# Kernel optimization log

Measured on AMD Instinct MI355X. Metric: run time of the kernel, lower is better.

The kernel has to match this reference:

```python
import jax, jax.numpy as jnp
import numpy as np

B, L = 1024, 50
H = 512
N_ITEM, N_ENTITY, N_WORD = 50000, 100000, 30000


def setup_inputs() -> dict:
    key = jax.random.key(0)
    ks = jax.random.split(key, 16)
    inp = {
        "item_ids": jax.random.randint(ks[0], (B, L), 0, N_ITEM),
        "item_len": jax.random.randint(ks[1], (B,), 0, 51),
        "entity_ids": jax.random.randint(ks[2], (B, L), 0, N_ENTITY),
        "entity_len": jax.random.randint(ks[3], (B,), 0, 51),
        "word_ids": jax.random.randint(ks[4], (B, L), 0, N_WORD),
        "word_len": jax.random.randint(ks[5], (B,), 0, 51),
        "labels": jax.random.randint(ks[6], (B,), 0, N_ITEM),
        # learned parameters (torch default-ish init scales)
        "item_emb": jax.random.normal(ks[7], (N_ITEM, H), jnp.float32),
        "entity_emb": jax.random.normal(ks[8], (N_ENTITY, H), jnp.float32),
        "word_emb": jax.random.normal(ks[9], (N_WORD, H), jnp.float32),
        "W1": jax.random.normal(ks[10], (H, 4 * H), jnp.float32) / np.sqrt(H),
        "b1": jnp.zeros((4 * H,), jnp.float32),
        "W2": jax.random.normal(ks[11], (4 * H, N_ITEM), jnp.float32) / np.sqrt(4 * H),
        "b2": jnp.zeros((N_ITEM,), jnp.float32),
    }
    return inp


def _masked_mean(table, ids, lens):
    # segment-mean over ragged lists encoded as padded ids + lengths.
    # empty list -> zeros (matches the torch zero-fallback branch).
    mask = (jnp.arange(L)[None, :] < lens[:, None]).astype(table.dtype)  # [B,L]
    emb = table[ids]                                                     # [B,L,H]
    s = jnp.einsum("blh,bl->bh", emb, mask)
    denom = jnp.maximum(lens, 1).astype(table.dtype)[:, None]
    return s / denom


def reference(item_emb, entity_emb, word_emb, W1, b1, W2, b2,
              item_ids, item_len, entity_ids, entity_len,
              word_ids, word_len, labels):
    u = (_masked_mean(item_emb, item_ids, item_len)
         + _masked_mean(entity_emb, entity_ids, entity_len)
         + _masked_mean(word_emb, word_ids, word_len)) / 3.0   # [B,H]
    h = jax.nn.relu(u @ W1 + b1)                                # [B,4H]
    probs = jax.nn.softmax(h @ W2 + b2, axis=-1)                # [B,n_item]
    # faithful to source: CrossEntropyLoss applied on top of softmax outputs
    logp = jax.nn.log_softmax(probs, axis=-1)
    loss = -jnp.mean(jnp.take_along_axis(logp, labels[:, None], axis=-1))
    return probs, labels, loss
```

## Files before the change

### kernel.cpp

```cpp
#include <hip/hip_runtime.h>
#include <cstdint>
#include <cstddef>

typedef __attribute__((ext_vector_type(8))) short bf16x8;
typedef __attribute__((ext_vector_type(4))) float f32x4;

#define B_DIM 1024
#define L_SEQ 50
#define H_DIM 512
#define NITEM 50000
#define PSTRIDE 400

__device__ __forceinline__ unsigned short f2bf(float x) {
  unsigned u = __float_as_uint(x);
  return (unsigned short)((u + 0x7fffu + ((u >> 16) & 1u)) >> 16);
}
__device__ __forceinline__ unsigned pack2(float lo, float hi) {
  return (unsigned)f2bf(lo) | ((unsigned)f2bf(hi) << 16);
}
__device__ __forceinline__ void gld16(const unsigned short* g, unsigned short* l) {
  __builtin_amdgcn_global_load_lds((const __attribute__((address_space(1))) void*)g,
                                   (__attribute__((address_space(3))) void*)l, 16, 0, 0);
}
#define BAR() asm volatile("s_barrier" ::: "memory")

__device__ __forceinline__ void mean_body(int b2, const int* __restrict__ item_ids,
                                          const int* __restrict__ item_len,
                                          const int* __restrict__ ent_ids,
                                          const int* __restrict__ ent_len,
                                          const int* __restrict__ word_ids,
                                          const int* __restrict__ word_len,
                                          const float* __restrict__ item_emb,
                                          const float* __restrict__ ent_emb,
                                          const float* __restrict__ word_emb,
                                          unsigned short* __restrict__ u_bf) {
  const int b = b2 >> 1;
  const int col = ((b2 & 1) << 8) + threadIdx.x;
  float out = 0.f;
  {
    const int len = item_len[b]; float a = 0.f;
#pragma unroll 4
    for (int l = 0; l < len; ++l) a += item_emb[(size_t)item_ids[b * L_SEQ + l] * H_DIM + col];
    out += a / (float)(len > 0 ? len : 1);
  }
  {
    const int len = ent_len[b]; float a = 0.f;
#pragma unroll 4
    for (int l = 0; l < len; ++l) a += ent_emb[(size_t)ent_ids[b * L_SEQ + l] * H_DIM + col];
    out += a / (float)(len > 0 ? len : 1);
  }
  {
    const int len = word_len[b]; float a = 0.f;
#pragma unroll 4
    for (int l = 0; l < len; ++l) a += word_emb[(size_t)word_ids[b * L_SEQ + l] * H_DIM + col];
    out += a / (float)(len > 0 ? len : 1);
  }
  u_bf[b * H_DIM + col] = f2bf(out / 3.f);
}

__global__ void mean_kernel(const int* __restrict__ item_ids, const int* __restrict__ item_len,
                            const int* __restrict__ ent_ids, const int* __restrict__ ent_len,
                            const int* __restrict__ word_ids, const int* __restrict__ word_len,
                            const float* __restrict__ item_emb, const float* __restrict__ ent_emb,
                            const float* __restrict__ word_emb, unsigned short* __restrict__ u_bf) {
  mean_body(blockIdx.x, item_ids, item_len, ent_ids, ent_len, word_ids, word_len, item_emb,
            ent_emb, word_emb, u_bf);
}

__device__ __forceinline__ void transpose_body(const float* __restrict__ W,
                                               unsigned short* __restrict__ Wt, int K, int N,
                                               int k0, int n0, float (*tile)[65]) {
  const int tn = threadIdx.x & 63, tk = threadIdx.x >> 6;
  const int nv = (n0 + tn < N) ? n0 + tn : N - 1;
#pragma unroll
  for (int i = 0; i < 16; ++i)
    tile[tk + 4 * i][tn] = W[(size_t)(k0 + tk + 4 * i) * N + nv];
  __syncthreads();
  const int rn = threadIdx.x >> 2, ck = (threadIdx.x & 3) * 16;
  if (n0 + rn < N) {
    uint4 o[2];
    unsigned* po = (unsigned*)&o[0];
#pragma unroll
    for (int c = 0; c < 8; ++c)
      po[c] = pack2(tile[ck + 2 * c][rn], tile[ck + 2 * c + 1][rn]);
    *(uint4*)&Wt[(size_t)(n0 + rn) * K + k0 + ck] = o[0];
    *(uint4*)&Wt[(size_t)(n0 + rn) * K + k0 + ck + 8] = o[1];
  }
}

__global__ void prep_kernel(const int* __restrict__ item_ids, const int* __restrict__ item_len,
                            const int* __restrict__ ent_ids, const int* __restrict__ ent_len,
                            const int* __restrict__ word_ids, const int* __restrict__ word_len,
                            const float* __restrict__ item_emb, const float* __restrict__ ent_emb,
                            const float* __restrict__ word_emb, unsigned short* __restrict__ u_bf,
                            const float* __restrict__ W1, unsigned short* __restrict__ W1t,
                            const float* __restrict__ W2, unsigned short* __restrict__ W2t) {
  __shared__ float tile[64][65];
  const int b = blockIdx.x;
  if (b < 2048) {
    mean_body(b, item_ids, item_len, ent_ids, ent_len, word_ids, word_len, item_emb, ent_emb,
              word_emb, u_bf);
  } else if (b < 2048 + 25024) {
    const int t = b - 2048;
    transpose_body(W2, W2t, 2048, NITEM, (t & 31) * 64, (t >> 5) * 64, tile);
  } else {
    const int t = b - (2048 + 25024);
    transpose_body(W1, W1t, 512, 2048, (t & 7) * 64, (t >> 3) * 64, tile);
  }
}

template <int K, int N>
__global__ void transpose_bf16(const float* __restrict__ W, unsigned short* __restrict__ Wt) {
  __shared__ float tile[64][65];
  transpose_body(W, Wt, K, N, blockIdx.x * 64, blockIdx.y * 64, tile);
}

template <int K, int N, int EPI>
__global__ __launch_bounds__(512, 1) void gemm128x256(const unsigned short* __restrict__ Ag,
                                                      const unsigned short* __restrict__ Btg,
                                                      const float* __restrict__ bias,
                                                      unsigned short* __restrict__ Cbf,
                                                      float* __restrict__ Cf,
                                                      float* __restrict__ pmax,
                                                      float* __restrict__ psum) {
  __shared__ unsigned short lds[4 * 4096 + 4 * 8192];
  unsigned short* Aring = lds;
  unsigned short* Bring = lds + 4 * 4096;

  const int tid = threadIdx.x;
  const int lane = tid & 63;
  const int wid = tid >> 6;

  const int nwg = gridDim.x;
  const int wgid = (blockIdx.x & 7) * (nwg >> 3) + (blockIdx.x >> 3);
  const int m0 = (wgid & 7) * 128;
  const int panel = wgid >> 3;
  const int n0 = panel * 256;

  const int cg = (lane & 3) ^ ((lane >> 3) & 3);
  const int arow = wid * 16 + (lane >> 2);
  const unsigned short* pa = Ag + (size_t)(m0 + arow) * K + cg * 8;
  const int br0 = wid * 32 + (lane >> 2), br1 = br0 + 16;
  int rg0 = n0 + br0; rg0 = rg0 < N ? rg0 : N - 1;
  int rg1 = n0 + br1; rg1 = rg1 < N ? rg1 : N - 1;
  const unsigned short* pb0 = Btg + (size_t)rg0 * K + cg * 8;
  const unsigned short* pb1 = Btg + (size_t)rg1 * K + cg * 8;
  const int li0 = wid * 2, li1 = wid * 2 + 1;

  const int wr = wid >> 2, wc = wid & 3;
  const int l15 = lane & 15, kb = lane >> 4;
  f32x4 acc[4][4] = {};

  const int HS = K / 32;
#pragma unroll
  for (int hh = 0; hh < 3; ++hh) {
    const int ko = hh * 32;
    gld16(pa + ko, &Aring[hh * 4096 + wid * 512]);
    gld16(pb0 + ko, &Bring[hh * 8192 + li0 * 512]);
    gld16(pb1 + ko, &Bring[hh * 8192 + li1 * 512]);
  }
  asm volatile("s_waitcnt vmcnt(6)" ::: "memory");
  BAR();

#pragma unroll 1
  for (int h = 0; h < HS; ++h) {
    const int slot = h & 3;
    const int nslot = (h + 3) & 3;
    const int kst = (h + 3) * 32;
    const unsigned short* As_ = &Aring[slot * 4096];
    const unsigned short* Bs_ = &Bring[slot * 8192];

    if (h + 3 < HS) {
      gld16(pa + kst, &Aring[nslot * 4096 + wid * 512]);
      gld16(pb0 + kst, &Bring[nslot * 8192 + li0 * 512]);
      gld16(pb1 + kst, &Bring[nslot * 8192 + li1 * 512]);
    }

    bf16x8 af[4], bf[4];
#pragma unroll
    for (int i = 0; i < 4; ++i) {
      const int row = wr * 64 + i * 16 + l15;
      af[i] = *(const bf16x8*)&As_[row * 32 + (kb ^ ((row >> 1) & 3)) * 8];
    }
#pragma unroll
    for (int j = 0; j < 4; ++j) {
      const int col = wc * 64 + j * 16 + l15;
      bf[j] = *(const bf16x8*)&Bs_[col * 32 + (kb ^ ((col >> 1) & 3)) * 8];
    }
    __builtin_amdgcn_s_setprio(1);
#pragma unroll
    for (int i = 0; i < 4; ++i)
#pragma unroll
      for (int j = 0; j < 4; ++j)
        acc[i][j] = __builtin_amdgcn_mfma_f32_16x16x32_bf16(af[i], bf[j], acc[i][j], 0, 0, 0);
    __builtin_amdgcn_s_setprio(0);

    if (h + 1 < HS) {
      if (h + 4 <= HS)
        asm volatile("s_waitcnt vmcnt(6)" ::: "memory");
      else if (h + 3 == HS)
        asm volatile("s_waitcnt vmcnt(3)" ::: "memory");
      else
        asm volatile("s_waitcnt vmcnt(0)" ::: "memory");
      BAR();
    }
  }

  float bv[4];
  bool val[4];
#pragma unroll
  for (int j = 0; j < 4; ++j) {
    const int cgl = n0 + wc * 64 + 16 * j + l15;
    val[j] = (cgl < N);
    bv[j] = bias[val[j] ? cgl : 0];
  }
#pragma unroll
  for (int i = 0; i < 4; ++i) {
    const int rbase = m0 + wr * 64 + 16 * i + 4 * kb;
#pragma unroll
    for (int j = 0; j < 4; ++j) {
      if (val[j]) {
        const int cgl = n0 + wc * 64 + 16 * j + l15;
#pragma unroll
        for (int rr = 0; rr < 4; ++rr) {
          const float v = acc[i][j][rr] + bv[j];
          if (EPI == 0)
            Cbf[(size_t)(rbase + rr) * N + cgl] = f2bf(v > 0.f ? v : 0.f);
          else
            Cf[(size_t)(rbase + rr) * N + cgl] = v;
        }
      }
    }
  }

  if constexpr (EPI == 1) {
    __syncthreads();
    float* redm = (float*)&lds[0];
    float* reds = redm + 512;
#pragma unroll
    for (int i = 0; i < 4; ++i) {
#pragma unroll
      for (int rr = 0; rr < 4; ++rr) {
        float mx = -3.0e38f;
#pragma unroll
        for (int j = 0; j < 4; ++j)
          if (val[j]) mx = fmaxf(mx, acc[i][j][rr] + bv[j]);
#pragma unroll
        for (int d = 1; d < 16; d <<= 1) mx = fmaxf(mx, __shfl_xor(mx, d));
        float s = 0.f;
#pragma unroll
        for (int j = 0; j < 4; ++j)
          if (val[j]) s += expf(acc[i][j][rr] + bv[j] - mx);
#pragma unroll
        for (int d = 1; d < 16; d <<= 1) s += __shfl_xor(s, d);
        if (l15 == 0) {
          const int rw = wr * 64 + 16 * i + 4 * kb + rr;
          redm[wc * 128 + rw] = mx;
          reds[wc * 128 + rw] = s;
        }
      }
    }
    __syncthreads();
    if (tid < 128) {
      float mm = redm[tid], ss = reds[tid];
#pragma unroll
      for (int w = 1; w < 4; ++w) {
        const float ma = redm[w * 128 + tid], sa = reds[w * 128 + tid];
        const float nm = fmaxf(mm, ma);
        ss = ss * expf(mm - nm) + sa * expf(ma - nm);
        mm = nm;
      }
      pmax[(size_t)(m0 + tid) * PSTRIDE + panel] = mm;
      psum[(size_t)(m0 + tid) * PSTRIDE + panel] = ss;
    }
  }
}

template <int K, int N, int EPI>
__global__ __launch_bounds__(256, 2) void gemm128(const unsigned short* __restrict__ Ag,
                                                  const unsigned short* __restrict__ Btg,
                                                  const float* __restrict__ bias,
                                                  unsigned short* __restrict__ Cbf,
                                                  float* __restrict__ Cf) {
  __shared__ unsigned short As[2][128 * 64];
  __shared__ unsigned short Bs[2][128 * 64];
  const int tid = threadIdx.x;
  const int lane = tid & 63;
  const int wid = tid >> 6;
  const int nwg = gridDim.x;
  const int wgid = (blockIdx.x & 7) * (nwg >> 3) + (blockIdx.x >> 3);
  const int m0 = (wgid & 7) * 128;
  const int n0 = (wgid >> 3) * 128;
  const int srsub = lane >> 3;
  const int scg = (lane & 7) ^ srsub;
  const unsigned short* pa[4];
  const unsigned short* pb[4];
#pragma unroll
  for (int qq = 0; qq < 4; ++qq) {
    const int seg = wid * 4 + qq;
    const int row = seg * 8 + srsub;
    pa[qq] = Ag + (size_t)(m0 + row) * K + scg * 8;
    int rg = n0 + row;
    rg = rg < N ? rg : N - 1;
    pb[qq] = Btg + (size_t)rg * K + scg * 8;
  }
  auto stage = [&](int t, int s) {
    const int ko = t * 64;
#pragma unroll
    for (int qq = 0; qq < 4; ++qq) {
      const int seg = wid * 4 + qq;
      gld16(pa[qq] + ko, &As[s][seg * 512]);
      gld16(pb[qq] + ko, &Bs[s][seg * 512]);
    }
  };
  const int wr = wid >> 1, wc = wid & 1;
  const int l15 = lane & 15, kb = lane >> 4;
  f32x4 acc[4][4] = {};
  auto compute = [&](int s) {
#pragma unroll
    for (int koi = 0; koi < 2; ++koi) {
      bf16x8 af[4], bf[4];
#pragma unroll
      for (int i = 0; i < 4; ++i) {
        const int row = wr * 64 + i * 16 + l15;
        af[i] = *(const bf16x8*)&As[s][row * 64 + ((koi * 4 + kb) ^ (row & 7)) * 8];
      }
#pragma unroll
      for (int j = 0; j < 4; ++j) {
        const int col = wc * 64 + j * 16 + l15;
        bf[j] = *(const bf16x8*)&Bs[s][col * 64 + ((koi * 4 + kb) ^ (col & 7)) * 8];
      }
#pragma unroll
      for (int i = 0; i < 4; ++i)
#pragma unroll
        for (int j = 0; j < 4; ++j)
          acc[i][j] = __builtin_amdgcn_mfma_f32_16x16x32_bf16(af[i], bf[j], acc[i][j], 0, 0, 0);
    }
  };
  const int NT = K / 64;
  stage(0, 0);
  asm volatile("s_waitcnt vmcnt(0)" ::: "memory");
  __syncthreads();
#pragma unroll 1
  for (int t = 0; t < NT; ++t) {
    if (t + 1 < NT) stage(t + 1, (t + 1) & 1);
    compute(t & 1);
    asm volatile("s_waitcnt vmcnt(0)" ::: "memory");
    __syncthreads();
  }
  float bv[4];
  bool val[4];
#pragma unroll
  for (int j = 0; j < 4; ++j) {
    const int cg2 = n0 + wc * 64 + 16 * j + l15;
    val[j] = (cg2 < N);
    bv[j] = bias[val[j] ? cg2 : 0];
  }
#pragma unroll
  for (int i = 0; i < 4; ++i) {
    const int rbase = m0 + wr * 64 + 16 * i + 4 * kb;
#pragma unroll
    for (int j = 0; j < 4; ++j) {
      if (val[j]) {
        const int cg2 = n0 + wc * 64 + 16 * j + l15;
#pragma unroll
        for (int rr = 0; rr < 4; ++rr) {
          const float v = acc[i][j][rr] + bv[j];
          if (EPI == 0)
            Cbf[(size_t)(rbase + rr) * N + cg2] = f2bf(v > 0.f ? v : 0.f);
          else
            Cf[(size_t)(rbase + rr) * N + cg2] = v;
        }
      }
    }
  }
}

template <int K, int N, int EPI>
__global__ __launch_bounds__(512, 2) void gemm_fused(const unsigned short* __restrict__ Ag,
                                                     const float* __restrict__ Bg,
                                                     const float* __restrict__ bias,
                                                     unsigned short* __restrict__ Cbf,
                                                     float* __restrict__ Cf,
                                                     float* __restrict__ pmax,
                                                     float* __restrict__ psum) {
  __shared__ unsigned short As[2][256 * 64];
  __shared__ uint4 Bs[2][8 * 128];
  const int tid = threadIdx.x;
  const int lane = tid & 63;
  const int wid = tid >> 6;
  const int m0 = blockIdx.x * 256;
  const int n0 = blockIdx.y * 128;
  const int arow = tid >> 3;
  const int ach = tid & 7;
  const int bn = 2 * lane;
  const int bk = 8 * wid;
  const int bcolg = (n0 + bn < N - 2) ? (n0 + bn) : (N - 2);
  uint4 areg[4];
  float2 breg[8];
  f32x4 acc[4][4] = {};
  auto stage_global = [&](int kt) {
    const int k0 = kt * 64;
#pragma unroll
    for (int qq = 0; qq < 4; ++qq)
      areg[qq] = *(const uint4*)&Ag[(size_t)(m0 + arow + 64 * qq) * K + k0 + 8 * ach];
#pragma unroll
    for (int i = 0; i < 8; ++i) breg[i] = *(const float2*)&Bg[(size_t)(k0 + bk + i) * N + bcolg];
  };
  auto stage_lds = [&](int buf) {
#pragma unroll
    for (int qq = 0; qq < 4; ++qq) {
      const int row = arow + 64 * qq;
      *(uint4*)&As[buf][row * 64 + ((8 * ach) ^ ((row & 7) * 8))] = areg[qq];
    }
    uint4 c0, c1;
    c0.x = pack2(breg[0].x, breg[1].x); c0.y = pack2(breg[2].x, breg[3].x);
    c0.z = pack2(breg[4].x, breg[5].x); c0.w = pack2(breg[6].x, breg[7].x);
    c1.x = pack2(breg[0].y, breg[1].y); c1.y = pack2(breg[2].y, breg[3].y);
    c1.z = pack2(breg[4].y, breg[5].y); c1.w = pack2(breg[6].y, breg[7].y);
    Bs[buf][wid * 128 + bn] = c0;
    Bs[buf][wid * 128 + bn + 1] = c1;
  };
  const int wr = wid & 3, wc = wid >> 2;
  const int mw = 64 * wr, nw = 64 * wc;
  const int l15 = lane & 15, kb = lane >> 4;
  auto compute = [&](int buf) {
#pragma unroll
    for (int koi = 0; koi < 2; ++koi) {
      bf16x8 af[4], bfv[4];
#pragma unroll
      for (int i = 0; i < 4; ++i) {
        const int row = mw + 16 * i + l15;
        af[i] = *(const bf16x8*)&As[buf][row * 64 + ((32 * koi + 8 * kb) ^ ((row & 7) * 8))];
      }
#pragma unroll
      for (int j = 0; j < 4; ++j)
        bfv[j] = *(const bf16x8*)&Bs[buf][(4 * koi + kb) * 128 + nw + 16 * j + l15];
#pragma unroll
      for (int i = 0; i < 4; ++i)
#pragma unroll
        for (int j = 0; j < 4; ++j)
          acc[i][j] = __builtin_amdgcn_mfma_f32_16x16x32_bf16(af[i], bfv[j], acc[i][j], 0, 0, 0);
    }
  };
  const int NT = K / 64;
  stage_global(0);
  stage_lds(0);
  __syncthreads();
  for (int t = 0; t < NT; ++t) {
    const int cur = t & 1;
    if (t + 1 < NT) stage_global(t + 1);
    compute(cur);
    if (t + 1 < NT) stage_lds(cur ^ 1);
    __syncthreads();
  }
  float bv[4];
  bool val[4];
#pragma unroll
  for (int j = 0; j < 4; ++j) {
    const int cg2 = n0 + nw + 16 * j + l15;
    val[j] = (cg2 < N);
    bv[j] = bias[val[j] ? cg2 : 0];
  }
#pragma unroll
  for (int i = 0; i < 4; ++i) {
    const int rbase = m0 + mw + 16 * i + 4 * kb;
#pragma unroll
    for (int j = 0; j < 4; ++j) {
      if (val[j]) {
        const int cg2 = n0 + nw + 16 * j + l15;
#pragma unroll
        for (int rr = 0; rr < 4; ++rr) {
          const float v = acc[i][j][rr] + bv[j];
          if (EPI == 0)
            Cbf[(size_t)(rbase + rr) * N + cg2] = f2bf(v > 0.f ? v : 0.f);
          else
            Cf[(size_t)(rbase + rr) * N + cg2] = v;
        }
      }
    }
  }
  if constexpr (EPI == 1) {
    float* redm = (float*)&As[0][0];
    float* reds = redm + 512;
#pragma unroll
    for (int i = 0; i < 4; ++i) {
#pragma unroll
      for (int rr = 0; rr < 4; ++rr) {
        float mx = -3.0e38f;
#pragma unroll
        for (int j = 0; j < 4; ++j)
          if (val[j]) mx = fmaxf(mx, acc[i][j][rr] + bv[j]);
#pragma unroll
        for (int d = 1; d < 16; d <<= 1) mx = fmaxf(mx, __shfl_xor(mx, d));
        float s = 0.f;
#pragma unroll
        for (int j = 0; j < 4; ++j)
          if (val[j]) s += expf(acc[i][j][rr] + bv[j] - mx);
#pragma unroll
        for (int d = 1; d < 16; d <<= 1) s += __shfl_xor(s, d);
        if (l15 == 0) {
          const int rl = mw + 16 * i + 4 * kb + rr;
          redm[wc * 256 + rl] = mx;
          reds[wc * 256 + rl] = s;
        }
      }
    }
    __syncthreads();
    if (tid < 256) {
      const float ma = redm[tid], mb = redm[256 + tid];
      const float mm = fmaxf(ma, mb);
      const float ss = reds[tid] * expf(ma - mm) + reds[256 + tid] * expf(mb - mm);
      pmax[(size_t)(m0 + tid) * PSTRIDE + blockIdx.y] = mm;
      psum[(size_t)(m0 + tid) * PSTRIDE + blockIdx.y] = ss;
    }
  }
}

__global__ void smax1r(const float* __restrict__ pmax, const float* __restrict__ psum,
                       float* __restrict__ rms, int ntiles) {
  const int b = blockIdx.x;
  const int l = threadIdx.x;
  float m = -3.4e38f, s = 0.f;
  for (int i = l; i < ntiles; i += 64) {
    const float pm = pmax[(size_t)b * PSTRIDE + i];
    const float ps = psum[(size_t)b * PSTRIDE + i];
    const float nm = fmaxf(m, pm);
    s = s * expf(m - nm) + ps * expf(pm - nm);
    m = nm;
  }
  for (int d = 1; d < 64; d <<= 1) {
    const float om = __shfl_xor(m, d), os = __shfl_xor(s, d);
    const float nm = fmaxf(m, om);
    s = s * expf(m - nm) + os * expf(om - nm);
    m = nm;
  }
  if (l == 0) {
    rms[b] = m;
    rms[B_DIM + b] = s;
  }
}

__global__ void smax2(float* __restrict__ buf, const float* __restrict__ rms,
                      const int* __restrict__ labels, float* __restrict__ row_lp) {
  const int b = blockIdx.x;
  float4* p = (float4*)(buf + (size_t)b * NITEM);
  const float m = rms[b];
  const float inv = 1.f / rms[B_DIM + b];
  const int lab = labels[b];
  __shared__ float s_pl;
  __shared__ float ss[256];
  float s2 = 0.f;
  for (int i = threadIdx.x; i < NITEM / 4; i += 256) {
    const float4 v = p[i];
    float pr[4];
#pragma unroll
    for (int j = 0; j < 4; ++j) {
      pr[j] = expf((&v.x)[j] - m) * inv;
      s2 += expf(pr[j] - inv);
    }
    float4 w;
    w.x = pr[0]; w.y = pr[1]; w.z = pr[2]; w.w = pr[3];
    p[i] = w;
    if ((lab >> 2) == i) s_pl = pr[lab & 3];
  }
  ss[threadIdx.x] = s2;
  __syncthreads();
  for (int off = 128; off > 0; off >>= 1) {
    if (threadIdx.x < off) ss[threadIdx.x] += ss[threadIdx.x + off];
    __syncthreads();
  }
  if (threadIdx.x == 0) row_lp[b] = s_pl - (inv + logf(ss[0]));
}

__global__ void fin(const float* __restrict__ row_lp, const int* __restrict__ labels,
                    float* __restrict__ out) {
  __shared__ float sb[256];
  float a = 0.f;
  for (int i = threadIdx.x; i < B_DIM; i += 256) {
    a += row_lp[i];
    out[(size_t)B_DIM * NITEM + i] = (float)labels[i];
  }
  sb[threadIdx.x] = a;
  __syncthreads();
  for (int off = 128; off > 0; off >>= 1) {
    if (threadIdx.x < off) sb[threadIdx.x] += sb[threadIdx.x + off];
    __syncthreads();
  }
  if (threadIdx.x == 0) out[(size_t)B_DIM * NITEM + B_DIM] = -sb[0] / (float)B_DIM;
}

extern "C" void kernel_launch(void* const* d_in, const int* in_sizes, int n_in,
                              void* d_out, int out_size, void* d_ws, size_t ws_size,
                              hipStream_t stream) {
  const int* item_ids = (const int*)d_in[0];
  const int* item_len = (const int*)d_in[1];
  const int* ent_ids = (const int*)d_in[2];
  const int* ent_len = (const int*)d_in[3];
  const int* word_ids = (const int*)d_in[4];
  const int* word_len = (const int*)d_in[5];
  const int* labels = (const int*)d_in[6];
  const float* item_emb = (const float*)d_in[7];
  const float* ent_emb = (const float*)d_in[8];
  const float* word_emb = (const float*)d_in[9];
  const float* W1 = (const float*)d_in[10];
  const float* b1 = (const float*)d_in[11];
  const float* W2 = (const float*)d_in[12];
  const float* b2 = (const float*)d_in[13];

  float* out = (float*)d_out;
  char* ws = (char*)d_ws;
  unsigned short* u_bf = (unsigned short*)ws;
  unsigned short* h_bf = (unsigned short*)(ws + (1 << 20));
  float* pmax = (float*)(ws + 5 * (1 << 20));
  float* psum = (float*)(ws + 7 * (1 << 20));
  float* rms = (float*)(ws + 9 * (1 << 20));
  float* row_lp = rms + 2 * B_DIM;
  unsigned short* W1t = (unsigned short*)(ws + 10 * (1 << 20));
  unsigned short* W2t = (unsigned short*)(ws + 16 * (1 << 20));
  float* logits = out;

  const size_t need = (size_t)16 * (1 << 20) + (size_t)NITEM * 2048 * 2;
  const bool fast = ws_size >= need;

  if (fast) {
    prep_kernel<<<2048 + 25024 + 256, 256, 0, stream>>>(item_ids, item_len, ent_ids, ent_len,
                                                        word_ids, word_len, item_emb, ent_emb,
                                                        word_emb, u_bf, W1, W1t, W2, W2t);
    gemm128<512, 2048, 0><<<8 * 16, 256, 0, stream>>>(u_bf, W1t, b1, h_bf, nullptr);
    gemm128x256<2048, NITEM, 1><<<8 * 196, 512, 0, stream>>>(h_bf, W2t, b2, nullptr, logits,
                                                             pmax, psum);
    smax1r<<<B_DIM, 64, 0, stream>>>(pmax, psum, rms, 196);
  } else {
    mean_kernel<<<2 * B_DIM, 256, 0, stream>>>(item_ids, item_len, ent_ids, ent_len, word_ids,
                                               word_len, item_emb, ent_emb, word_emb, u_bf);
    gemm_fused<512, 2048, 0><<<dim3(4, 16), 512, 0, stream>>>(u_bf, W1, b1, h_bf, nullptr,
                                                              nullptr, nullptr);
    gemm_fused<2048, NITEM, 1><<<dim3(4, 391), 512, 0, stream>>>(h_bf, W2, b2, nullptr, logits,
                                                                 pmax, psum);
    smax1r<<<B_DIM, 64, 0, stream>>>(pmax, psum, rms, 391);
  }
  smax2<<<B_DIM, 256, 0, stream>>>(logits, rms, labels, row_lp);
  fin<<<1, 256, 0, stream>>>(row_lp, labels, out);
}
```

Baseline: 618.8 us.

## Use 256x256 tiles for the main output GEMM with 128x256 tail kernel

Adds a 256x256-tile GEMM kernel for the large logits GEMM that covers the first 192 column panels with 768 workgroups, and handles the remaining 4 panels with the existing 128x256 kernel through a new panel-offset template parameter. Larger tiles double the reuse of each loaded B tile and cut global/LDS traffic per MFMA. In exchange it uses more accumulator registers, a larger LDS ring, and an extra kernel launch for the tail, and the coarser grid may balance less evenly across the CUs.

```diff
diff --git a/kernel.cpp b/kernel.cpp
--- a/kernel.cpp
+++ b/kernel.cpp
@@ -109,13 +109,191 @@
   }
 }
 
-template <int K, int N>
-__global__ void transpose_bf16(const float* __restrict__ W, unsigned short* __restrict__ Wt) {
-  __shared__ float tile[64][65];
-  transpose_body(W, Wt, K, N, blockIdx.x * 64, blockIdx.y * 64, tile);
-}
-
 template <int K, int N, int EPI>
+__global__ __launch_bounds__(512, 1) void gemm256k(const unsigned short* __restrict__ Ag,
+                                                   const unsigned short* __restrict__ Btg,
+                                                   const float* __restrict__ bias,
+                                                   unsigned short* __restrict__ Cbf,
+                                                   float* __restrict__ Cf,
+                                                   float* __restrict__ pmax,
+                                                   float* __restrict__ psum) {
+  __shared__ unsigned short lds[8 * 8192];
+  unsigned short* Aring = lds;
+  unsigned short* Bring = lds + 4 * 8192;
+
+  const int tid = threadIdx.x;
+  const int lane = tid & 63;
+  const int wid = tid >> 6;
+
+  const int nwg = gridDim.x;
+  const int wgid = (blockIdx.x & 7) * (nwg >> 3) + (blockIdx.x >> 3);
+  const int m0 = (wgid & 3) * 256;
+  const int panel = wgid >> 2;
+  const int n0 = panel * 256;
+
+  const int r0 = (wid * 2) * 16 + (lane >> 2);
+  const int r1 = r0 + 16;
+  const int cg = (lane & 3) ^ ((lane >> 3) & 3);
+  const unsigned short* pa0 = Ag + (size_t)(m0 + r0) * K + cg * 8;
+  const unsigned short* pa1 = Ag + (size_t)(m0 + r1) * K + cg * 8;
+  int rg0 = n0 + r0; rg0 = rg0 < N ? rg0 : N - 1;
+  int rg1 = n0 + r1; rg1 = rg1 < N ? rg1 : N - 1;
+  const unsigned short* pb0 = Btg + (size_t)rg0 * K + cg * 8;
+  const unsigned short* pb1 = Btg + (size_t)rg1 * K + cg * 8;
+  const int li0 = wid * 2, li1 = wid * 2 + 1;
+
+  const int wr = wid >> 2, wc = wid & 3;
+  const int l15 = lane & 15, kb = lane >> 4;
+  f32x4 acc[8][4] = {};
+
+  const int HS = K / 32;
+#pragma unroll
+  for (int hh = 0; hh < 3; ++hh) {
+    const int ko = hh * 32, sl = hh & 3;
+    gld16(pa0 + ko, &Aring[sl * 8192 + li0 * 512]);
+    gld16(pa1 + ko, &Aring[sl * 8192 + li1 * 512]);
+    gld16(pb0 + ko, &Bring[sl * 8192 + li0 * 512]);
+    gld16(pb1 + ko, &Bring[sl * 8192 + li1 * 512]);
+  }
+  asm volatile("s_waitcnt vmcnt(8)" ::: "memory");
+  BAR();
+
+#pragma unroll 1
+  for (int h = 0; h < HS; ++h) {
+    const int slot = h & 3;
+    const int nslot = (h + 3) & 3;
+    const int kst = (h + 3) * 32;
+    const bool st = (h + 3) < HS;
+    const unsigned short* As_ = &Aring[slot * 8192];
+    const unsigned short* Bs_ = &Bring[slot * 8192];
+
+    bf16x8 afA[4], bfr[4];
+#pragma unroll
+    for (int i = 0; i < 4; ++i) {
+      const int row = wr * 128 + i * 16 + l15;
+      afA[i] = *(const bf16x8*)&As_[row * 32 + (kb ^ ((row >> 1) & 3)) * 8];
+    }
+#pragma unroll
+    for (int j = 0; j < 4; ++j) {
+      const int col = wc * 64 + j * 16 + l15;
+      bfr[j] = *(const bf16x8*)&Bs_[col * 32 + (kb ^ ((col >> 1) & 3)) * 8];
+    }
+    if (st) {
+      gld16(pa0 + kst, &Aring[nslot * 8192 + li0 * 512]);
+      gld16(pa1 + kst, &Aring[nslot * 8192 + li1 * 512]);
+    }
+    BAR();
+    __builtin_amdgcn_s_setprio(1);
+#pragma unroll
+    for (int i = 0; i < 4; ++i)
+#pragma unroll
+      for (int j = 0; j < 4; ++j)
+        acc[i][j] = __builtin_amdgcn_mfma_f32_16x16x32_bf16(afA[i], bfr[j], acc[i][j], 0, 0, 0);
+    __builtin_amdgcn_s_setprio(0);
+    BAR();
+
+    bf16x8 afB[4];
+#pragma unroll
+    for (int i = 0; i < 4; ++i) {
+      const int row = wr * 128 + (i + 4) * 16 + l15;
+      afB[i] = *(const bf16x8*)&As_[row * 32 + (kb ^ ((row >> 1) & 3)) * 8];
+    }
+    if (st) {
+      gld16(pb0 + kst, &Bring[nslot * 8192 + li0 * 512]);
+      gld16(pb1 + kst, &Bring[nslot * 8192 + li1 * 512]);
+    }
+    BAR();
+    __builtin_amdgcn_s_setprio(1);
+#pragma unroll
+    for (int i = 0; i < 4; ++i)
+#pragma unroll
+      for (int j = 0; j < 4; ++j)
+        acc[i + 4][j] =
+            __builtin_amdgcn_mfma_f32_16x16x32_bf16(afB[i], bfr[j], acc[i + 4][j], 0, 0, 0);
+    __builtin_amdgcn_s_setprio(0);
+
+    if (h + 1 < HS) {
+      if (h + 4 <= HS)
+        asm volatile("s_waitcnt vmcnt(8)" ::: "memory");
+      else if (h + 3 == HS)
+        asm volatile("s_waitcnt vmcnt(4)" ::: "memory");
+      else
+        asm volatile("s_waitcnt vmcnt(0)" ::: "memory");
+      BAR();
+    }
+  }
+
+  float bv[4];
+  bool val[4];
+#pragma unroll
+  for (int j = 0; j < 4; ++j) {
+    const int cgl = n0 + wc * 64 + 16 * j + l15;
+    val[j] = (cgl < N);
+    bv[j] = bias[val[j] ? cgl : 0];
+  }
+#pragma unroll
+  for (int i = 0; i < 8; ++i) {
+    const int rbase = m0 + wr * 128 + 16 * i + 4 * kb;
+#pragma unroll
+    for (int j = 0; j < 4; ++j) {
+      if (val[j]) {
+        const int cgl = n0 + wc * 64 + 16 * j + l15;
+#pragma unroll
+        for (int rr = 0; rr < 4; ++rr) {
+          const float v = acc[i][j][rr] + bv[j];
+          if (EPI == 0)
+            Cbf[(size_t)(rbase + rr) * N + cgl] = f2bf(v > 0.f ? v : 0.f);
+          else
+            Cf[(size_t)(rbase + rr) * N + cgl] = v;
+        }
+      }
+    }
+  }
+
+  if constexpr (EPI == 1) {
+    __syncthreads();
+    float* redm = (float*)&lds[0];
+    float* reds = redm + 1024;
+#pragma unroll
+    for (int i = 0; i < 8; ++i) {
+#pragma unroll
+      for (int rr = 0; rr < 4; ++rr) {
+        float mx = -3.0e38f;
+#pragma unroll
+        for (int j = 0; j < 4; ++j)
+          if (val[j]) mx = fmaxf(mx, acc[i][j][rr] + bv[j]);
+#pragma unroll
+        for (int d = 1; d < 16; d <<= 1) mx = fmaxf(mx, __shfl_xor(mx, d));
+        float s = 0.f;
+#pragma unroll
+        for (int j = 0; j < 4; ++j)
+          if (val[j]) s += expf(acc[i][j][rr] + bv[j] - mx);
+#pragma unroll
+        for (int d = 1; d < 16; d <<= 1) s += __shfl_xor(s, d);
+        if (l15 == 0) {
+          const int rw = wr * 128 + 16 * i + 4 * kb + rr;
+          redm[wc * 256 + rw] = mx;
+          reds[wc * 256 + rw] = s;
+        }
+      }
+    }
+    __syncthreads();
+    if (tid < 256) {
+      float mm = redm[tid], ss = reds[tid];
+#pragma unroll
+      for (int w = 1; w < 4; ++w) {
+        const float ma = redm[w * 256 + tid], sa = reds[w * 256 + tid];
+        const float nm = fmaxf(mm, ma);
+        ss = ss * expf(mm - nm) + sa * expf(ma - nm);
+        mm = nm;
+      }
+      pmax[(size_t)(m0 + tid) * PSTRIDE + panel] = mm;
+      psum[(size_t)(m0 + tid) * PSTRIDE + panel] = ss;
+    }
+  }
+}
+
+template <int K, int N, int EPI, int PBASE>
 __global__ __launch_bounds__(512, 1) void gemm128x256(const unsigned short* __restrict__ Ag,
                                                       const unsigned short* __restrict__ Btg,
                                                       const float* __restrict__ bias,
@@ -135,7 +313,7 @@
   const int wgid = (blockIdx.x & 7) * (nwg >> 3) + (blockIdx.x >> 3);
   const int m0 = (wgid & 7) * 128;
   const int panel = wgid >> 3;
-  const int n0 = panel * 256;
+  const int n0 = (PBASE + panel) * 256;
 
   const int cg = (lane & 3) ^ ((lane >> 3) & 3);
   const int arow = wid * 16 + (lane >> 2);
@@ -270,8 +448,8 @@
         ss = ss * expf(mm - nm) + sa * expf(ma - nm);
         mm = nm;
       }
-      pmax[(size_t)(m0 + tid) * PSTRIDE + panel] = mm;
-      psum[(size_t)(m0 + tid) * PSTRIDE + panel] = ss;
+      pmax[(size_t)(m0 + tid) * PSTRIDE + PBASE + panel] = mm;
+      psum[(size_t)(m0 + tid) * PSTRIDE + PBASE + panel] = ss;
     }
   }
 }
@@ -628,7 +806,9 @@
                                                         word_ids, word_len, item_emb, ent_emb,
                                                         word_emb, u_bf, W1, W1t, W2, W2t);
     gemm128<512, 2048, 0><<<8 * 16, 256, 0, stream>>>(u_bf, W1t, b1, h_bf, nullptr);
-    gemm128x256<2048, NITEM, 1><<<8 * 196, 512, 0, stream>>>(h_bf, W2t, b2, nullptr, logits,
+    gemm256k<2048, NITEM, 1><<<768, 512, 0, stream>>>(h_bf, W2t, b2, nullptr, logits, pmax,
+                                                      psum);
+    gemm128x256<2048, NITEM, 1, 192><<<32, 512, 0, stream>>>(h_bf, W2t, b2, nullptr, logits,
                                                              pmax, psum);
     smax1r<<<B_DIM, 64, 0, stream>>>(pmax, psum, rms, 196);
   } else {
```

Measured after the change: 562.3 us, median of 2. 1.1x faster.
